# Performance work log

Measured on AMD Instinct MI355X. Metric: run time of the kernel, lower is better.

## Reference

```python
import jax, jax.numpy as jnp
import numpy as np

EPS = 1e-5  # BatchNorm2d default eps


def _conv3x3(x, w):
    # x: [B,C,H,W], w: [O,I,3,3], stride 1, 'same' padding (autopad k=3 -> p=1)
    return jax.lax.conv_general_dilated(
        x, w, window_strides=(1, 1), padding=((1, 1), (1, 1)),
        dimension_numbers=("NCHW", "OIHW", "NCHW"))


def _bn(x, g, b, m, v):
    # inference-mode BatchNorm2d with materialized running stats
    scale = (g / jnp.sqrt(v + EPS))[None, :, None, None]
    return (x - m[None, :, None, None]) * scale + b[None, :, None, None]


def _silu(x):
    return x * jax.nn.sigmoid(x)


def _pam(y, q_w, q_b, k_w, k_b, v_w, v_b, pam_gamma):
    # PAM_Module: full pixel-wise self-attention over N = H*W tokens
    B, C, H, W = y.shape
    N = H * W
    yf = y.reshape(B, C, N)
    # 1x1 convs expressed as channel matmuls; q_w: [C//8, C], v_w: [C, C]
    q = jnp.einsum("oc,bcn->bno", q_w, yf) + q_b                 # [B, N, C//8]
    k = jnp.einsum("oc,bcn->bon", k_w, yf) + k_b[None, :, None]  # [B, C//8, N]
    v = jnp.einsum("oc,bcn->bon", v_w, yf) + v_b[None, :, None]  # [B, C, N]
    energy = jnp.einsum("bno,bom->bnm", q, k)                    # [B, N, N]
    attn = jax.nn.softmax(energy, axis=-1)
    # torch: bmm(v, attn.permute(0,2,1)) -> out[b,c,n] = sum_m v[b,c,m] * attn[b,n,m]
    out = jnp.einsum("bcm,bnm->bcn", v, attn).reshape(B, C, H, W)
    return pam_gamma * out + y


def setup_inputs() -> dict:
    key = jax.random.key(0)
    ks = jax.random.split(key, 16)
    B, C1, C2, H, W = 4, 64, 64, 64, 64
    C_ = C2 // 2          # e = 0.5
    C8 = C2 // 8          # PAM q/k channels
    s = 0.05
    inp = {
        "x": jax.random.normal(ks[0], (B, C1, H, W), jnp.float32),
        # cv1: Conv(c1, c_, 3, 1)
        "cv1_w": jax.random.normal(ks[1], (C_, C1, 3, 3), jnp.float32) * s,
        "bn1_g": jax.random.uniform(ks[2], (C_,), jnp.float32, 0.5, 1.5),
        "bn1_b": jax.random.normal(ks[3], (C_,), jnp.float32) * s,
        "bn1_m": jax.random.normal(ks[4], (C_,), jnp.float32) * s,
        "bn1_v": jax.random.uniform(ks[5], (C_,), jnp.float32, 0.5, 1.5),
        # cv2: Conv(c_, c2, 3, 1)
        "cv2_w": jax.random.normal(ks[6], (C2, C_, 3, 3), jnp.float32) * s,
        "bn2_g": jax.random.uniform(ks[7], (C2,), jnp.float32, 0.5, 1.5),
        "bn2_b": jax.random.normal(ks[8], (C2,), jnp.float32) * s,
        "bn2_m": jax.random.normal(ks[9], (C2,), jnp.float32) * s,
        "bn2_v": jax.random.uniform(ks[10], (C2,), jnp.float32, 0.5, 1.5),
        # PAM 1x1 convs (flattened kernels) + biases + gamma
        "q_w": jax.random.normal(ks[11], (C8, C2), jnp.float32) * s,
        "q_b": jax.random.normal(ks[12], (C8,), jnp.float32) * s,
        "k_w": jax.random.normal(ks[13], (C8, C2), jnp.float32) * s,
        "k_b": jax.random.normal(ks[14], (C8,), jnp.float32) * s,
        "v_w": jax.random.normal(ks[15], (C2, C2), jnp.float32) * s,
        "v_b": jnp.zeros((C2,), jnp.float32),
        "pam_gamma": jnp.float32(0.5),  # torch inits 0 (identity); nonzero to exercise path
    }
    return inp


def reference(x, cv1_w, bn1_g, bn1_b, bn1_m, bn1_v,
              cv2_w, bn2_g, bn2_b, bn2_m, bn2_v,
              q_w, q_b, k_w, k_b, v_w, v_b, pam_gamma):
    y = _silu(_bn(_conv3x3(x, cv1_w), bn1_g, bn1_b, bn1_m, bn1_v))   # cv1
    y = _silu(_bn(_conv3x3(y, cv2_w), bn2_g, bn2_b, bn2_m, bn2_v))   # cv2
    # SAA: PAM applied twice on identical input and summed == 2 * PAM(y)
    att = 2.0 * _pam(y, q_w, q_b, k_w, k_b, v_w, v_b, pam_gamma)
    return x + att  # shortcut active (c1 == c2)
```

## Files before the change

kernel.cpp:

```cpp
#include <hip/hip_runtime.h>
#include <hip/hip_bf16.h>

#define NB 4
#define NN 4096

typedef short  bf16x8 __attribute__((ext_vector_type(8)));
typedef float  f32x4  __attribute__((ext_vector_type(4)));

static __device__ __forceinline__ ushort f2bf(float f) {
    unsigned u = __float_as_uint(f);
    u += 0x7fffu + ((u >> 16) & 1u);
    return (ushort)(u >> 16);
}

__global__ __launch_bounds__(256) void prep(
    const float* __restrict__ x, const float* __restrict__ w1, const float* __restrict__ w2,
    ushort* __restrict__ xt, ushort* __restrict__ W1r, ushort* __restrict__ W2r)
{
    const int tid = threadIdx.x;
    const int blk = blockIdx.x;
    if (blk < 256) {
        __shared__ float Ts[64][66];
        const int b = blk >> 6, n0 = (blk & 63) * 64;
        const int wv = tid >> 6, lane = tid & 63;
        #pragma unroll
        for (int i = 0; i < 16; ++i) {
            int ci = i * 4 + wv, nn = lane;
            Ts[ci][nn] = x[((size_t)b * 64 + ci) * NN + n0 + nn];
        }
        __syncthreads();
        #pragma unroll
        for (int i = 0; i < 16; ++i) {
            int nn = i * 4 + wv, ci = lane;
            xt[((size_t)b * NN + n0 + nn) * 64 + ci] = f2bf(Ts[ci][nn]);
        }
    } else if (blk < 258) {
        const int base = (blk - 256) * 9216;
        #pragma unroll
        for (int i = 0; i < 36; ++i) {
            int e = base + i * 256 + tid;
            int co = e / 576, k = e % 576, tap = k >> 6, ci = k & 63;
            W1r[e] = f2bf(w1[((size_t)co * 64 + ci) * 9 + tap]);
        }
    } else {
        const int base = (blk - 258) * 9216;
        #pragma unroll
        for (int i = 0; i < 36; ++i) {
            int e = base + i * 256 + tid;
            int co = e / 288, k = e % 288, tap = k >> 5, ci = k & 31;
            W2r[e] = f2bf(w2[((size_t)co * 32 + ci) * 9 + tap]);
        }
    }
}

__global__ __launch_bounds__(256) void conv1_mfma(
    const ushort* __restrict__ xt, const ushort* __restrict__ W1r,
    const float* __restrict__ bng, const float* __restrict__ bnb,
    const float* __restrict__ bnm, const float* __restrict__ bnv,
    ushort* __restrict__ y1t)
{
    __shared__ __align__(16) ushort As[32 * 600];
    __shared__ __align__(16) ushort Xs[24 * 66 * 8];

    const int tid = threadIdx.x;
    const int h = blockIdx.x, b = blockIdx.y;

    #pragma unroll
    for (int i = 0; i < 9; ++i) {
        int cid = i * 256 + tid;
        int row = cid / 72, off = cid % 72;
        *(uint4*)&As[row * 600 + off * 8] = *(const uint4*)(W1r + (size_t)cid * 8);
    }
    #pragma unroll
    for (int r = 0; r < 3; ++r) {
        int gh = h - 1 + r;
        #pragma unroll
        for (int i = 0; i < 2; ++i) {
            int cid = i * 256 + tid;
            int w_ = cid >> 3, cc = cid & 7;
            uint4 v = {0, 0, 0, 0};
            if ((unsigned)gh < 64u)
                v = *(const uint4*)(xt + ((size_t)(b * NN + gh * 64) * 64) + (size_t)cid * 8);
            *(uint4*)&Xs[((r * 8 + cc) * 66 + (w_ + 1)) * 8] = v;
        }
    }
    if (tid < 48) {
        int r = tid >> 4, q = tid & 15, cc = q >> 1, side = (q & 1) * 65;
        uint4 z = {0, 0, 0, 0};
        *(uint4*)&Xs[((r * 8 + cc) * 66 + side) * 8] = z;
    }
    __syncthreads();

    const int lane = tid & 63, wv = tid >> 6;
    const int quad = lane >> 4, l15 = lane & 15;
    const int ch = wv & 1, ph = wv >> 1;

    f32x4 acc[2] = {{0.f,0.f,0.f,0.f},{0.f,0.f,0.f,0.f}};
    #pragma unroll
    for (int kk = 0; kk < 18; ++kk) {
        const int tap = kk >> 1;
        const int dyr = tap / 3, dx = tap % 3;
        bf16x8 af = *(const bf16x8*)&As[(ch * 16 + l15) * 600 + kk * 32 + quad * 8];
        #pragma unroll
        for (int s = 0; s < 2; ++s) {
            int p = ph * 32 + s * 16 + l15;
            bf16x8 bf = *(const bf16x8*)&Xs[((dyr * 8 + (kk & 1) * 4 + quad) * 66 + p + dx) * 8];
            acc[s] = __builtin_amdgcn_mfma_f32_16x16x32_bf16(af, bf, acc[s], 0, 0, 0);
        }
    }

    const int cb = ch * 16 + quad * 4;
    float sc[4], bs[4];
    #pragma unroll
    for (int r = 0; r < 4; ++r) {
        int co = cb + r;
        sc[r] = bng[co] / sqrtf(bnv[co] + 1e-5f);
        bs[r] = bnb[co] - bnm[co] * sc[r];
    }
    #pragma unroll
    for (int s = 0; s < 2; ++s) {
        int p = ph * 32 + s * 16 + l15;
        ushort u4[4];
        #pragma unroll
        for (int r = 0; r < 4; ++r) {
            float pre = acc[s][r] * sc[r] + bs[r];
            u4[r] = f2bf(pre / (1.f + __expf(-pre)));
        }
        *(uint2*)&y1t[((size_t)(b * NN + h * 64 + p)) * 32 + cb] = *(uint2*)u4;
    }
}

__global__ __launch_bounds__(256) void conv2qkv(
    const ushort* __restrict__ y1t, const ushort* __restrict__ W2r,
    const float* __restrict__ bng, const float* __restrict__ bnb,
    const float* __restrict__ bnm, const float* __restrict__ bnv,
    const float* __restrict__ qw, const float* __restrict__ qb,
    const float* __restrict__ kw, const float* __restrict__ kb,
    const float* __restrict__ vw, const float* __restrict__ vb,
    float* __restrict__ y, ushort* __restrict__ q8,
    ushort* __restrict__ ko, ushort* __restrict__ vt)
{
    __shared__ __align__(16) ushort As[64 * 312];
    __shared__ __align__(16) ushort Xs[12 * 66 * 8];
    __shared__ __align__(16) ushort Yt[64 * 76];
    __shared__ __align__(16) ushort Wq[80 * 76];
    __shared__ float Bv[80];

    const int tid = threadIdx.x;
    const int h = blockIdx.x, b = blockIdx.y;

    #pragma unroll
    for (int i = 0; i < 9; ++i) {
        int cid = i * 256 + tid;
        int row = cid / 36, off = cid % 36;
        *(uint4*)&As[row * 312 + off * 8] = *(const uint4*)(W2r + (size_t)cid * 8);
    }
    #pragma unroll
    for (int r = 0; r < 3; ++r) {
        int gh = h - 1 + r;
        int cid = tid;
        int w_ = cid >> 2, cc = cid & 3;
        uint4 v = {0, 0, 0, 0};
        if ((unsigned)gh < 64u)
            v = *(const uint4*)(y1t + ((size_t)(b * NN + gh * 64) * 32) + (size_t)cid * 8);
        *(uint4*)&Xs[((r * 4 + cc) * 66 + (w_ + 1)) * 8] = v;
    }
    if (tid < 24) {
        int r = tid >> 3, q = tid & 7, cc = q >> 1, side = (q & 1) * 65;
        uint4 z = {0, 0, 0, 0};
        *(uint4*)&Xs[((r * 4 + cc) * 66 + side) * 8] = z;
    }
    for (int i = tid; i < 2560; i += 256) {
        int chw = i >> 5, c2 = (i & 31) * 2;
        const float* src = (chw < 8) ? (qw + chw * 64 + c2)
                         : (chw < 16) ? (kw + (chw - 8) * 64 + c2)
                         : (vw + (chw - 16) * 64 + c2);
        float2 v2 = *(const float2*)src;
        *(unsigned*)&Wq[chw * 76 + c2] = ((unsigned)f2bf(v2.y) << 16) | f2bf(v2.x);
    }
    if (tid < 80) Bv[tid] = (tid < 8) ? qb[tid] : (tid < 16) ? kb[tid - 8] : vb[tid - 16];
    __syncthreads();

    const int lane = tid & 63, wv = tid >> 6;
    const int quad = lane >> 4, l15 = lane & 15;

    f32x4 acc[4] = {{0.f,0.f,0.f,0.f},{0.f,0.f,0.f,0.f},{0.f,0.f,0.f,0.f},{0.f,0.f,0.f,0.f}};
    #pragma unroll
    for (int kk = 0; kk < 9; ++kk) {
        const int dyr = kk / 3, dx = kk % 3;
        bf16x8 af = *(const bf16x8*)&As[(wv * 16 + l15) * 312 + kk * 32 + quad * 8];
        #pragma unroll
        for (int s = 0; s < 4; ++s) {
            int p = s * 16 + l15;
            bf16x8 bf = *(const bf16x8*)&Xs[((dyr * 4 + quad) * 66 + p + dx) * 8];
            acc[s] = __builtin_amdgcn_mfma_f32_16x16x32_bf16(af, bf, acc[s], 0, 0, 0);
        }
    }

    const int cb = wv * 16 + quad * 4;
    float sc[4], bs[4];
    #pragma unroll
    for (int r = 0; r < 4; ++r) {
        int co = cb + r;
        sc[r] = bng[co] / sqrtf(bnv[co] + 1e-5f);
        bs[r] = bnb[co] - bnm[co] * sc[r];
    }
    #pragma unroll
    for (int s = 0; s < 4; ++s) {
        int p = s * 16 + l15;
        #pragma unroll
        for (int r = 0; r < 4; ++r) {
            float pre = acc[s][r] * sc[r] + bs[r];
            float res = pre / (1.f + __expf(-pre));
            y[((size_t)(b * 64 + cb + r)) * NN + h * 64 + p] = res;
            Yt[p * 76 + cb + r] = f2bf(res);
        }
    }
    __syncthreads();

    bf16x8 aY0 = *(const bf16x8*)&Yt[(wv * 16 + l15) * 76 + quad * 8];
    bf16x8 aY1 = *(const bf16x8*)&Yt[(wv * 16 + l15) * 76 + 32 + quad * 8];
    const int nbase = h * 64 + wv * 16 + quad * 4;
    const int vtile = h * 2 + (wv >> 1);
    const int vslot = quad * 8 + (wv & 1) * 4;
    #pragma unroll
    for (int cht = 0; cht < 5; ++cht) {
        bf16x8 bW0 = *(const bf16x8*)&Wq[(cht * 16 + l15) * 76 + quad * 8];
        bf16x8 bW1 = *(const bf16x8*)&Wq[(cht * 16 + l15) * 76 + 32 + quad * 8];
        f32x4 qa = {0.f, 0.f, 0.f, 0.f};
        qa = __builtin_amdgcn_mfma_f32_16x16x32_bf16(aY0, bW0, qa, 0, 0, 0);
        qa = __builtin_amdgcn_mfma_f32_16x16x32_bf16(aY1, bW1, qa, 0, 0, 0);
        const float bias = Bv[cht * 16 + l15];
        const int chn = cht * 16 + l15;
        if (cht == 0) {
            if (l15 < 8) {
                #pragma unroll
                for (int r = 0; r < 4; ++r)
                    q8[((size_t)b * NN + nbase + r) * 8 + chn] = f2bf(qa[r] + bias);
            } else {
                #pragma unroll
                for (int r = 0; r < 4; ++r)
                    ko[((size_t)b * NN + nbase + r) * 8 + (chn - 8)] = f2bf(qa[r] + bias);
            }
        } else {
            const int c = chn - 16;
            ushort u4[4];
            #pragma unroll
            for (int r = 0; r < 4; ++r) u4[r] = f2bf(qa[r] + bias);
            *(uint2*)&vt[(((size_t)(b * 128 + vtile)) * 64 + c) * 32 + vslot] = *(uint2*)u4;
        }
    }
}

__global__ __launch_bounds__(512, 4) void flash_pam(
    const ushort* __restrict__ q8,
    const ushort* __restrict__ k8,
    const ushort* __restrict__ vt,
    const float* __restrict__ y,
    const float* __restrict__ x,
    const float* __restrict__ gamma_p,
    float* __restrict__ out)
{
    __shared__ __align__(16) float Osum[4 * 2304];
    __shared__ float Lw[8][32];
    __shared__ float Ls[32];

    const int tid = threadIdx.x;
    const int bx = blockIdx.x;
    const int b  = bx >> 7;
    const int nt = bx & 127;
    const int n0 = nt * 32;

    const int lane = tid & 63, w = tid >> 6;
    const int quad = lane >> 4, l15 = lane & 15;

    const uint4 z4 = {0u, 0u, 0u, 0u};

    bf16x8 bQ[2];
    #pragma unroll
    for (int af = 0; af < 2; ++af) {
        uint4 qv = *(const uint4*)(q8 + ((size_t)b * NN + n0 + af * 16 + l15) * 8);
        uint4 sel = (quad == 0) ? qv : z4;
        bQ[af] = *(bf16x8*)&sel;
    }

    const ushort* kg = k8 + ((size_t)b * NN + w * 512) * 8;
    const ushort* vg = vt + ((size_t)(b * 128 + w * 16)) * 64 * 32;

    f32x4 acc[2][4] = {{{0.f,0.f,0.f,0.f},{0.f,0.f,0.f,0.f},{0.f,0.f,0.f,0.f},{0.f,0.f,0.f,0.f}},
                       {{0.f,0.f,0.f,0.f},{0.f,0.f,0.f,0.f},{0.f,0.f,0.f,0.f},{0.f,0.f,0.f,0.f}}};
    float lacc[2] = {0.f, 0.f};
    const f32x4 zf = {0.f, 0.f, 0.f, 0.f};

    #pragma unroll 2
    for (int t = 0; t < 16; ++t) {
        const int g = t * 32;
        uint4 k0r = *(const uint4*)(kg + (size_t)(g + l15) * 8);
        uint4 k1r = *(const uint4*)(kg + (size_t)(g + 16 + l15) * 8);
        uint4 k0s = (quad == 0) ? k0r : z4;
        uint4 k1s = (quad == 0) ? k1r : z4;
        bf16x8 aK0 = *(bf16x8*)&k0s;
        bf16x8 aK1 = *(bf16x8*)&k1s;

        bf16x8 vb_[4];
        #pragma unroll
        for (int ct = 0; ct < 4; ++ct)
            vb_[ct] = *(const bf16x8*)(vg + (size_t)t * 2048 + (ct * 16 + l15) * 32 + quad * 8);

        f32x4 s0[2], s1[2];
        #pragma unroll
        for (int af = 0; af < 2; ++af) {
            s0[af] = __builtin_amdgcn_mfma_f32_16x16x32_bf16(aK0, bQ[af], zf, 0, 0, 0);
            s1[af] = __builtin_amdgcn_mfma_f32_16x16x32_bf16(aK1, bQ[af], zf, 0, 0, 0);
        }

        bf16x8 pa[2];
        #pragma unroll
        for (int af = 0; af < 2; ++af) {
            union { ushort u[8]; bf16x8 v; } pk;
            #pragma unroll
            for (int r = 0; r < 4; ++r) {
                float e = __expf(s0[af][r]);
                lacc[af] += e;
                pk.u[r] = f2bf(e);
            }
            #pragma unroll
            for (int r = 0; r < 4; ++r) {
                float e = __expf(s1[af][r]);
                lacc[af] += e;
                pk.u[4 + r] = f2bf(e);
            }
            pa[af] = pk.v;
        }

        #pragma unroll
        for (int af = 0; af < 2; ++af)
            #pragma unroll
            for (int ct = 0; ct < 4; ++ct)
                acc[af][ct] = __builtin_amdgcn_mfma_f32_16x16x32_bf16(pa[af], vb_[ct], acc[af][ct], 0, 0, 0);
    }

    #pragma unroll
    for (int af = 0; af < 2; ++af) {
        lacc[af] += __shfl_xor(lacc[af], 16, 64);
        lacc[af] += __shfl_xor(lacc[af], 32, 64);
    }
    if (quad == 0) {
        Lw[w][l15]      = lacc[0];
        Lw[w][16 + l15] = lacc[1];
    }

    if (w >= 4) {
        #pragma unroll
        for (int af = 0; af < 2; ++af)
            #pragma unroll
            for (int ct = 0; ct < 4; ++ct)
                *(f32x4*)&Osum[(w - 4) * 2304 + (ct * 16 + l15) * 36 + af * 16 + quad * 4] = acc[af][ct];
    }
    __syncthreads();
    if (w < 4) {
        #pragma unroll
        for (int af = 0; af < 2; ++af)
            #pragma unroll
            for (int ct = 0; ct < 4; ++ct) {
                float* p = &Osum[w * 2304 + (ct * 16 + l15) * 36 + af * 16 + quad * 4];
                f32x4 v = *(const f32x4*)p;
                *(f32x4*)p = v + acc[af][ct];
            }
    }
    if (tid < 32) Ls[tid] = Lw[0][tid] + Lw[1][tid] + Lw[2][tid] + Lw[3][tid]
                          + Lw[4][tid] + Lw[5][tid] + Lw[6][tid] + Lw[7][tid];
    __syncthreads();

    {
        const int c = tid >> 3, nn = (tid & 7) * 4;
        f32x4 o = {0.f, 0.f, 0.f, 0.f};
        #pragma unroll
        for (int s = 0; s < 4; ++s)
            o += *(const f32x4*)&Osum[s * 2304 + c * 36 + nn];
        const float g2 = 2.f * gamma_p[0];
        const size_t idx = ((size_t)b * 64 + c) * NN + n0 + nn;
        f32x4 xv = *(const f32x4*)(x + idx);
        f32x4 yv = *(const f32x4*)(y + idx);
        f32x4 res;
        #pragma unroll
        for (int u = 0; u < 4; ++u)
            res[u] = xv[u] + 2.f * yv[u] + g2 * o[u] / Ls[nn + u];
        *(f32x4*)(out + idx) = res;
    }
}

extern "C" void kernel_launch(void* const* d_in, const int* in_sizes, int n_in,
                              void* d_out, int out_size, void* d_ws, size_t ws_size,
                              hipStream_t stream) {
    const float* x    = (const float*)d_in[0];
    const float* w1   = (const float*)d_in[1];
    const float* g1   = (const float*)d_in[2];
    const float* b1   = (const float*)d_in[3];
    const float* m1   = (const float*)d_in[4];
    const float* v1   = (const float*)d_in[5];
    const float* w2   = (const float*)d_in[6];
    const float* g2   = (const float*)d_in[7];
    const float* b2   = (const float*)d_in[8];
    const float* m2   = (const float*)d_in[9];
    const float* v2   = (const float*)d_in[10];
    const float* qw   = (const float*)d_in[11];
    const float* qb   = (const float*)d_in[12];
    const float* kw   = (const float*)d_in[13];
    const float* kb   = (const float*)d_in[14];
    const float* vw   = (const float*)d_in[15];
    const float* vb   = (const float*)d_in[16];
    const float* gam  = (const float*)d_in[17];
    float* outp = (float*)d_out;

    float* ws = (float*)d_ws;
    ushort* xt  = (ushort*)ws;
    float*  y   = ws + 524288;
    ushort* q8  = (ushort*)(ws + 1572864);
    ushort* kk  = (ushort*)(ws + 1703936);
    ushort* vv  = (ushort*)(ws + 1769472);
    float*  S   = ws + 2326528;
    ushort* y1t = (ushort*)S;
    ushort* W1r = (ushort*)(S + 262144);
    ushort* W2r = (ushort*)(S + 271360);

    prep<<<260, 256, 0, stream>>>(x, w1, w2, xt, W1r, W2r);
    conv1_mfma<<<dim3(64, NB), 256, 0, stream>>>(xt, W1r, g1, b1, m1, v1, y1t);
    conv2qkv<<<dim3(64, NB), 256, 0, stream>>>(y1t, W2r, g2, b2, m2, v2,
                                               qw, qb, kw, kb, vw, vb,
                                               y, q8, kk, vv);
    flash_pam<<<512, 512, 0, stream>>>(q8, kk, vv, y, x, gam, outp);
}
```

Baseline: 133.5 us.

## Double query tile per flash_pam block and use packed bf16 conversions

flash_pam now handles 64 query positions per block instead of 32, with a 256-block grid. Each loaded K/V fragment therefore feeds twice as many MFMAs, which halves the K/V traffic across the grid. The softmax normaliser is turned into a reciprocal multiply, and the software bf16 rounding is replaced by the hardware v_cvt_pk_bf16_f32 instruction in conv1, conv2qkv and the attention loop. In exchange each block needs more registers and LDS, the launch bound drops to 2 blocks per CU, and the smaller grid may leave less parallelism to hide latency.

```diff
diff --git a/kernel.cpp b/kernel.cpp
--- a/kernel.cpp
+++ b/kernel.cpp
@@ -11,6 +11,12 @@
     unsigned u = __float_as_uint(f);
     u += 0x7fffu + ((u >> 16) & 1u);
     return (ushort)(u >> 16);
+}
+
+static __device__ __forceinline__ unsigned cvt_pk_bf16(float a, float b) {
+    unsigned r;
+    asm("v_cvt_pk_bf16_f32 %0, %1, %2" : "=v"(r) : "v"(a), "v"(b));
+    return r;
 }
 
 __global__ __launch_bounds__(256) void prep(
@@ -120,13 +126,16 @@
     #pragma unroll
     for (int s = 0; s < 2; ++s) {
         int p = ph * 32 + s * 16 + l15;
-        ushort u4[4];
+        float r_[4];
         #pragma unroll
         for (int r = 0; r < 4; ++r) {
             float pre = acc[s][r] * sc[r] + bs[r];
-            u4[r] = f2bf(pre / (1.f + __expf(-pre)));
-        }
-        *(uint2*)&y1t[((size_t)(b * NN + h * 64 + p)) * 32 + cb] = *(uint2*)u4;
+            r_[r] = pre / (1.f + __expf(-pre));
+        }
+        uint2 st;
+        st.x = cvt_pk_bf16(r_[0], r_[1]);
+        st.y = cvt_pk_bf16(r_[2], r_[3]);
+        *(uint2*)&y1t[((size_t)(b * NN + h * 64 + p)) * 32 + cb] = st;
     }
 }
 
@@ -176,7 +185,7 @@
                          : (chw < 16) ? (kw + (chw - 8) * 64 + c2)
                          : (vw + (chw - 16) * 64 + c2);
         float2 v2 = *(const float2*)src;
-        *(unsigned*)&Wq[chw * 76 + c2] = ((unsigned)f2bf(v2.y) << 16) | f2bf(v2.x);
+        *(unsigned*)&Wq[chw * 76 + c2] = cvt_pk_bf16(v2.x, v2.y);
     }
     if (tid < 80) Bv[tid] = (tid < 8) ? qb[tid] : (tid < 16) ? kb[tid - 8] : vb[tid - 16];
     __syncthreads();
@@ -244,15 +253,15 @@
             }
         } else {
             const int c = chn - 16;
-            ushort u4[4];
-            #pragma unroll
-            for (int r = 0; r < 4; ++r) u4[r] = f2bf(qa[r] + bias);
-            *(uint2*)&vt[(((size_t)(b * 128 + vtile)) * 64 + c) * 32 + vslot] = *(uint2*)u4;
-        }
-    }
-}
-
-__global__ __launch_bounds__(512, 4) void flash_pam(
+            uint2 st;
+            st.x = cvt_pk_bf16(qa[0] + bias, qa[1] + bias);
+            st.y = cvt_pk_bf16(qa[2] + bias, qa[3] + bias);
+            *(uint2*)&vt[(((size_t)(b * 128 + vtile)) * 64 + c) * 32 + vslot] = st;
+        }
+    }
+}
+
+__global__ __launch_bounds__(512, 2) void flash_pam(
     const ushort* __restrict__ q8,
     const ushort* __restrict__ k8,
     const ushort* __restrict__ vt,
@@ -261,24 +270,24 @@
     const float* __restrict__ gamma_p,
     float* __restrict__ out)
 {
-    __shared__ __align__(16) float Osum[4 * 2304];
-    __shared__ float Lw[8][32];
-    __shared__ float Ls[32];
+    __shared__ __align__(16) float Osum[4 * 4352];
+    __shared__ float Lw[8][64];
+    __shared__ float Ls[64];
 
     const int tid = threadIdx.x;
     const int bx = blockIdx.x;
-    const int b  = bx >> 7;
-    const int nt = bx & 127;
-    const int n0 = nt * 32;
+    const int b  = bx >> 6;
+    const int nt = bx & 63;
+    const int n0 = nt * 64;
 
     const int lane = tid & 63, w = tid >> 6;
     const int quad = lane >> 4, l15 = lane & 15;
 
     const uint4 z4 = {0u, 0u, 0u, 0u};
 
-    bf16x8 bQ[2];
-    #pragma unroll
-    for (int af = 0; af < 2; ++af) {
+    bf16x8 bQ[4];
+    #pragma unroll
+    for (int af = 0; af < 4; ++af) {
         uint4 qv = *(const uint4*)(q8 + ((size_t)b * NN + n0 + af * 16 + l15) * 8);
         uint4 sel = (quad == 0) ? qv : z4;
         bQ[af] = *(bf16x8*)&sel;
@@ -287,106 +296,109 @@
     const ushort* kg = k8 + ((size_t)b * NN + w * 512) * 8;
     const ushort* vg = vt + ((size_t)(b * 128 + w * 16)) * 64 * 32;
 
-    f32x4 acc[2][4] = {{{0.f,0.f,0.f,0.f},{0.f,0.f,0.f,0.f},{0.f,0.f,0.f,0.f},{0.f,0.f,0.f,0.f}},
-                       {{0.f,0.f,0.f,0.f},{0.f,0.f,0.f,0.f},{0.f,0.f,0.f,0.f},{0.f,0.f,0.f,0.f}}};
-    float lacc[2] = {0.f, 0.f};
+    f32x4 acc[4][4];
+    #pragma unroll
+    for (int af = 0; af < 4; ++af)
+        #pragma unroll
+        for (int ct = 0; ct < 4; ++ct)
+            acc[af][ct] = (f32x4){0.f, 0.f, 0.f, 0.f};
+    float lacc[4] = {0.f, 0.f, 0.f, 0.f};
     const f32x4 zf = {0.f, 0.f, 0.f, 0.f};
 
     #pragma unroll 2
     for (int t = 0; t < 16; ++t) {
         const int g = t * 32;
-        uint4 k0r = *(const uint4*)(kg + (size_t)(g + l15) * 8);
-        uint4 k1r = *(const uint4*)(kg + (size_t)(g + 16 + l15) * 8);
-        uint4 k0s = (quad == 0) ? k0r : z4;
-        uint4 k1s = (quad == 0) ? k1r : z4;
-        bf16x8 aK0 = *(bf16x8*)&k0s;
-        bf16x8 aK1 = *(bf16x8*)&k1s;
+        bf16x8 aK0 = *(const bf16x8*)(kg + (size_t)(g + l15) * 8);
+        bf16x8 aK1 = *(const bf16x8*)(kg + (size_t)(g + 16 + l15) * 8);
 
         bf16x8 vb_[4];
         #pragma unroll
         for (int ct = 0; ct < 4; ++ct)
             vb_[ct] = *(const bf16x8*)(vg + (size_t)t * 2048 + (ct * 16 + l15) * 32 + quad * 8);
 
-        f32x4 s0[2], s1[2];
-        #pragma unroll
-        for (int af = 0; af < 2; ++af) {
-            s0[af] = __builtin_amdgcn_mfma_f32_16x16x32_bf16(aK0, bQ[af], zf, 0, 0, 0);
-            s1[af] = __builtin_amdgcn_mfma_f32_16x16x32_bf16(aK1, bQ[af], zf, 0, 0, 0);
-        }
-
-        bf16x8 pa[2];
-        #pragma unroll
-        for (int af = 0; af < 2; ++af) {
-            union { ushort u[8]; bf16x8 v; } pk;
+        #pragma unroll
+        for (int af = 0; af < 4; ++af) {
+            f32x4 s0 = __builtin_amdgcn_mfma_f32_16x16x32_bf16(aK0, bQ[af], zf, 0, 0, 0);
+            f32x4 s1 = __builtin_amdgcn_mfma_f32_16x16x32_bf16(aK1, bQ[af], zf, 0, 0, 0);
+
+            float e[8];
             #pragma unroll
             for (int r = 0; r < 4; ++r) {
-                float e = __expf(s0[af][r]);
-                lacc[af] += e;
-                pk.u[r] = f2bf(e);
+                e[r]     = __expf(s0[r]);
+                e[4 + r] = __expf(s1[r]);
             }
             #pragma unroll
-            for (int r = 0; r < 4; ++r) {
-                float e = __expf(s1[af][r]);
-                lacc[af] += e;
-                pk.u[4 + r] = f2bf(e);
-            }
-            pa[af] = pk.v;
-        }
-
-        #pragma unroll
-        for (int af = 0; af < 2; ++af)
+            for (int r = 0; r < 8; ++r) lacc[af] += e[r];
+            union { unsigned u[4]; bf16x8 v; } pk;
+            pk.u[0] = cvt_pk_bf16(e[0], e[1]);
+            pk.u[1] = cvt_pk_bf16(e[2], e[3]);
+            pk.u[2] = cvt_pk_bf16(e[4], e[5]);
+            pk.u[3] = cvt_pk_bf16(e[6], e[7]);
+
             #pragma unroll
             for (int ct = 0; ct < 4; ++ct)
-                acc[af][ct] = __builtin_amdgcn_mfma_f32_16x16x32_bf16(pa[af], vb_[ct], acc[af][ct], 0, 0, 0);
-    }
-
-    #pragma unroll
-    for (int af = 0; af < 2; ++af) {
+                acc[af][ct] = __builtin_amdgcn_mfma_f32_16x16x32_bf16(pk.v, vb_[ct], acc[af][ct], 0, 0, 0);
+        }
+    }
+
+    #pragma unroll
+    for (int af = 0; af < 4; ++af) {
         lacc[af] += __shfl_xor(lacc[af], 16, 64);
         lacc[af] += __shfl_xor(lacc[af], 32, 64);
     }
     if (quad == 0) {
-        Lw[w][l15]      = lacc[0];
-        Lw[w][16 + l15] = lacc[1];
+        #pragma unroll
+        for (int af = 0; af < 4; ++af)
+            Lw[w][af * 16 + l15] = lacc[af];
     }
 
     if (w >= 4) {
         #pragma unroll
-        for (int af = 0; af < 2; ++af)
+        for (int af = 0; af < 4; ++af)
             #pragma unroll
             for (int ct = 0; ct < 4; ++ct)
-                *(f32x4*)&Osum[(w - 4) * 2304 + (ct * 16 + l15) * 36 + af * 16 + quad * 4] = acc[af][ct];
+                *(f32x4*)&Osum[(w - 4) * 4352 + (ct * 16 + l15) * 68 + af * 16 + quad * 4] = acc[af][ct];
     }
     __syncthreads();
     if (w < 4) {
         #pragma unroll
-        for (int af = 0; af < 2; ++af)
+        for (int af = 0; af < 4; ++af)
             #pragma unroll
             for (int ct = 0; ct < 4; ++ct) {
-                float* p = &Osum[w * 2304 + (ct * 16 + l15) * 36 + af * 16 + quad * 4];
+                float* p = &Osum[w * 4352 + (ct * 16 + l15) * 68 + af * 16 + quad * 4];
                 f32x4 v = *(const f32x4*)p;
                 *(f32x4*)p = v + acc[af][ct];
             }
     }
-    if (tid < 32) Ls[tid] = Lw[0][tid] + Lw[1][tid] + Lw[2][tid] + Lw[3][tid]
-                          + Lw[4][tid] + Lw[5][tid] + Lw[6][tid] + Lw[7][tid];
+    if (tid < 64) {
+        float s = Lw[0][tid] + Lw[1][tid] + Lw[2][tid] + Lw[3][tid]
+                + Lw[4][tid] + Lw[5][tid] + Lw[6][tid] + Lw[7][tid];
+        Ls[tid] = 1.0f / s;
+    }
     __syncthreads();
 
     {
-        const int c = tid >> 3, nn = (tid & 7) * 4;
-        f32x4 o = {0.f, 0.f, 0.f, 0.f};
-        #pragma unroll
-        for (int s = 0; s < 4; ++s)
-            o += *(const f32x4*)&Osum[s * 2304 + c * 36 + nn];
+        const int c = tid >> 3, n8 = (tid & 7) * 8;
+        f32x4 o0 = {0.f, 0.f, 0.f, 0.f}, o1 = {0.f, 0.f, 0.f, 0.f};
+        #pragma unroll
+        for (int s = 0; s < 4; ++s) {
+            o0 += *(const f32x4*)&Osum[s * 4352 + c * 68 + n8];
+            o1 += *(const f32x4*)&Osum[s * 4352 + c * 68 + n8 + 4];
+        }
         const float g2 = 2.f * gamma_p[0];
-        const size_t idx = ((size_t)b * 64 + c) * NN + n0 + nn;
-        f32x4 xv = *(const f32x4*)(x + idx);
-        f32x4 yv = *(const f32x4*)(y + idx);
-        f32x4 res;
-        #pragma unroll
-        for (int u = 0; u < 4; ++u)
-            res[u] = xv[u] + 2.f * yv[u] + g2 * o[u] / Ls[nn + u];
-        *(f32x4*)(out + idx) = res;
+        const size_t idx = ((size_t)b * 64 + c) * NN + n0 + n8;
+        f32x4 xv0 = *(const f32x4*)(x + idx);
+        f32x4 xv1 = *(const f32x4*)(x + idx + 4);
+        f32x4 yv0 = *(const f32x4*)(y + idx);
+        f32x4 yv1 = *(const f32x4*)(y + idx + 4);
+        f32x4 r0, r1;
+        #pragma unroll
+        for (int u = 0; u < 4; ++u) {
+            r0[u] = xv0[u] + 2.f * yv0[u] + g2 * o0[u] * Ls[n8 + u];
+            r1[u] = xv1[u] + 2.f * yv1[u] + g2 * o1[u] * Ls[n8 + 4 + u];
+        }
+        *(f32x4*)(out + idx) = r0;
+        *(f32x4*)(out + idx + 4) = r1;
     }
 }
 
@@ -429,5 +441,5 @@
     conv2qkv<<<dim3(64, NB), 256, 0, stream>>>(y1t, W2r, g2, b2, m2, v2,
                                                qw, qb, kw, kb, vw, vb,
                                                y, q8, kk, vv);
-    flash_pam<<<512, 512, 0, stream>>>(q8, kk, vv, y, x, gam, outp);
-}
+    flash_pam<<<256, 512, 0, stream>>>(q8, kk, vv, y, x, gam, outp);
+}
```

New measurement: 128.2 us. 4.0% less time.
